# Optimization experiments

Hardware: AMD Instinct MI355X
Metric: run time of the kernel (lower is better)

## Reference

```python
import jax, jax.numpy as jnp
import numpy as np

D_MODEL = 768
N_LAYER = 4
VOCAB = 10000
N_MELS = 80
D_STATE = 16
D_CONV = 4
DT_RANK = 48          # ceil(768/16)
D_INNER = 1536        # expand * d_model
B_SZ, L_SEQ = 2, 1024


def rmsnorm(x, w, eps=1e-5):
    return x * jax.lax.rsqrt(jnp.mean(x * x, axis=-1, keepdims=True) + eps) * w


def causal_depthwise_conv(x, w, b):
    # x: (b, l, d_inner); w: (d_inner, 1, d_conv); torch Conv1d with padding=d_conv-1, truncated to l
    xc = jax.lax.conv_general_dilated(
        jnp.transpose(x, (0, 2, 1)), w, window_strides=(1,),
        padding=[(D_CONV - 1, 0)], dimension_numbers=('NCH', 'OIH', 'NCH'),
        feature_group_count=D_INNER)
    xc = xc + b[None, :, None]
    return jnp.transpose(xc, (0, 2, 1))


def selective_scan(u, dt, A, B, C, D):
    # u, dt: (b,l,d_in); A: (d_in,n); B,C: (b,l,n); D: (d_in,)
    dA = jnp.einsum('bld,dn->bldn', dt, A)
    dB_u = jnp.einsum('bld,bld,bln->bldn', dt, u, B)
    dA = jnp.clip(dA, -20, None)
    # shift dA by one step (exclusive cumulative decay), cumsum mode
    dA_shift = jnp.pad(dA[:, 1:], ((0, 0), (1, 0), (0, 0), (0, 0)))
    dA_cumsum = jnp.exp(jnp.cumsum(dA_shift, axis=1))
    x = jnp.cumsum(dB_u / (dA_cumsum + 1e-12), axis=1) * dA_cumsum
    y = jnp.einsum('bldn,bln->bld', x, C)
    return y + u * D


def mamba_block(x, rms_w, in_w, cw, cb, xp_w, dt_w, dt_b, A_log, Dp, out_w):
    h = rmsnorm(x, rms_w)
    xz = h @ in_w                       # (b,l,2*d_inner)
    xi, res = jnp.split(xz, 2, axis=-1)
    xi = jax.nn.silu(causal_depthwise_conv(xi, cw, cb))
    A = -jnp.exp(A_log.astype(jnp.float32))
    x_dbl = xi @ xp_w                   # (b,l,dt_rank+2n)
    delta = x_dbl[..., :DT_RANK]
    Bm = x_dbl[..., DT_RANK:DT_RANK + D_STATE]
    Cm = x_dbl[..., DT_RANK + D_STATE:]
    delta = jax.nn.softplus(delta @ dt_w + dt_b)
    y = selective_scan(xi, delta, A, Bm, Cm, Dp.astype(jnp.float32))
    y = y * jax.nn.silu(res)
    return y @ out_w + x


def setup_inputs():
    key = jax.random.key(0)
    ks = jax.random.split(key, 8)
    s = 0.02
    return {
        'input_ids': jax.random.randint(ks[0], (B_SZ, L_SEQ), 0, VOCAB),
        'embedding': jax.random.normal(ks[1], (VOCAB, D_MODEL), jnp.float32) * s,
        'rms_w': jnp.ones((N_LAYER, D_MODEL), jnp.float32),
        'in_proj_w': jax.random.normal(ks[2], (N_LAYER, D_MODEL, 2 * D_INNER), jnp.float32) * s,
        'conv_w': jax.random.normal(ks[3], (N_LAYER, D_INNER, 1, D_CONV), jnp.float32) * 0.1,
        'conv_b': jnp.zeros((N_LAYER, D_INNER), jnp.float32),
        'x_proj_w': jax.random.normal(ks[4], (N_LAYER, D_INNER, DT_RANK + 2 * D_STATE), jnp.float32) * s,
        'dt_proj_w': jax.random.normal(ks[5], (N_LAYER, DT_RANK, D_INNER), jnp.float32) * s,
        'dt_proj_b': jnp.zeros((N_LAYER, D_INNER), jnp.float32),
        'A_log': jnp.broadcast_to(jnp.log(jnp.arange(1, D_STATE + 1, dtype=jnp.float32)), (N_LAYER, D_INNER, D_STATE)) + 0.0,
        'D_param': jnp.ones((N_LAYER, D_INNER), jnp.float32),
        'out_proj_w': jax.random.normal(ks[6], (N_LAYER, D_INNER, D_MODEL), jnp.float32) * s,
        'norm_f_w': jnp.ones((D_MODEL,), jnp.float32),
        'head_w': jax.random.normal(ks[7], (D_MODEL, N_MELS), jnp.float32) * s,
    }


def reference(input_ids, embedding, rms_w, in_proj_w, conv_w, conv_b, x_proj_w,
              dt_proj_w, dt_proj_b, A_log, D_param, out_proj_w, norm_f_w, head_w):
    x = embedding[input_ids]            # (b,l,d)
    for i in range(N_LAYER):
        x = mamba_block(x, rms_w[i], in_proj_w[i], conv_w[i], conv_b[i],
                        x_proj_w[i], dt_proj_w[i], dt_proj_b[i], A_log[i],
                        D_param[i], out_proj_w[i])
    x = rmsnorm(x, norm_f_w)
    return x @ head_w                   # (b,l,n_mels)
```

## Files before the change

### kernel.cpp

```cpp
#include <hip/hip_runtime.h>
#include <hip/hip_bf16.h>
#include <math.h>

#define D_MODEL 768
#define N_LAYER 4
#define D_STATE 16
#define D_CONV  4
#define DT_RANK 48
#define D_INNER 1536
#define B_SZ    2
#define L_SEQ   1024
#define N_MELS  80
#define ROWS    (B_SZ * L_SEQ)

typedef __bf16 bf16x8 __attribute__((ext_vector_type(8)));
typedef float  f32x4  __attribute__((ext_vector_type(4)));

__device__ __forceinline__ float fast_exp2(float x) {
    float r; asm("v_exp_f32 %0, %1" : "=v"(r) : "v"(x)); return r;
}
__device__ __forceinline__ float fast_exp(float x) {
    return fast_exp2(x * 1.44269504f);
}
__device__ __forceinline__ float fast_rcp(float x) {
    float r; asm("v_rcp_f32 %0, %1" : "=v"(r) : "v"(x)); return r;
}
__device__ __forceinline__ float silu_f(float v) {
    return v * fast_rcp(1.0f + fast_exp(-v));
}
__device__ __forceinline__ float softplus_f(float v) {
    return fmaxf(v, 0.0f) + log1pf(expf(-fabsf(v)));
}
__device__ __forceinline__ unsigned short f2bf(float f) {
    unsigned int u = __float_as_uint(f);
    unsigned int r = (u + 0x7FFFu + ((u >> 16) & 1u)) >> 16;
    return (unsigned short)r;
}
__device__ __forceinline__ float bf2f(unsigned short v) {
    return __uint_as_float(((unsigned int)v) << 16);
}

__global__ void embed_kernel(const int* __restrict__ ids,
                             const float* __restrict__ emb,
                             float* __restrict__ x) {
    int i = blockIdx.x * 256 + threadIdx.x;
    if (i >= ROWS * D_MODEL) return;
    int r = i / D_MODEL, c = i - r * D_MODEL;
    x[i] = emb[(size_t)ids[r] * D_MODEL + c];
}

__global__ void rmsnorm_kernel(const float* __restrict__ x,
                               const float* __restrict__ w,
                               unsigned short* __restrict__ hb) {
    int row = blockIdx.x;
    const float* xr = x + (size_t)row * D_MODEL;
    int tid = threadIdx.x;
    float p = 0.f;
    for (int c = tid; c < D_MODEL; c += 256) { float v = xr[c]; p = fmaf(v, v, p); }
    for (int off = 32; off >= 1; off >>= 1) p += __shfl_down(p, off, 64);
    __shared__ float ws[4];
    int lane = tid & 63, wv = tid >> 6;
    if (lane == 0) ws[wv] = p;
    __syncthreads();
    if (tid == 0) ws[0] = ws[0] + ws[1] + ws[2] + ws[3];
    __syncthreads();
    float scale = 1.0f / sqrtf(ws[0] / (float)D_MODEL + 1e-5f);
    for (int c = tid; c < D_MODEL; c += 256)
        hb[(size_t)row * D_MODEL + c] = f2bf(xr[c] * scale * w[c]);
}

__global__ void prep_weights_kernel(const float* __restrict__ in_wi,
                                    const float* __restrict__ out_wi,
                                    const float* __restrict__ xp_wi,
                                    const float* __restrict__ dt_wi,
                                    unsigned short* __restrict__ wt_in,
                                    unsigned short* __restrict__ wt_out,
                                    unsigned short* __restrict__ xpT,
                                    unsigned short* __restrict__ dtwT) {
    __shared__ float t[32][33];
    int bx = blockIdx.x;
    int tid = threadIdx.x;
    if (bx < 3456) {
        const float* src; unsigned short* dst; int R, C, cy, cx;
        if (bx < 2304) {
            src = in_wi; dst = wt_in; R = D_MODEL; C = 2 * D_INNER;
            cy = bx / 96; cx = bx - cy * 96;
        } else {
            int tt = bx - 2304;
            src = out_wi; dst = wt_out; R = D_INNER; C = D_MODEL;
            cy = tt / 24; cx = tt - cy * 24;
        }
        int tx = tid & 31, ty = tid >> 5;
        int r0 = cy * 32, c0 = cx * 32;
#pragma unroll
        for (int i = 0; i < 4; i++)
            t[ty + i * 8][tx] = src[(size_t)(r0 + ty + i * 8) * C + c0 + tx];
        __syncthreads();
#pragma unroll
        for (int i = 0; i < 4; i++)
            dst[(size_t)(c0 + ty + i * 8) * R + r0 + tx] = f2bf(t[tx][ty + i * 8]);
    } else {
        int i = (bx - 3456) * 256 + tid;
        if (i < 80 * D_INNER) {
            int c = i / D_INNER, r = i - c * D_INNER;
            xpT[i] = f2bf(xp_wi[(size_t)r * 80 + c]);
        } else {
            int i2 = i - 80 * D_INNER;
            int c = i2 >> 6, r = i2 & 63;
            dtwT[i2] = (r < DT_RANK) ? f2bf(dt_wi[(size_t)r * D_INNER + c])
                                     : (unsigned short)0;
        }
    }
}

__global__ void transpose_u16_kernel(const unsigned short* __restrict__ src,
                                     unsigned short* __restrict__ dst,
                                     int R, int C) {
    __shared__ unsigned short t[32][34];
    int tx = threadIdx.x & 31, ty = threadIdx.x >> 5;
    int r0 = blockIdx.y * 32, c0 = blockIdx.x * 32;
#pragma unroll
    for (int i = 0; i < 4; i++)
        t[ty + i * 8][tx] = src[(size_t)(r0 + ty + i * 8) * C + c0 + tx];
    __syncthreads();
#pragma unroll
    for (int i = 0; i < 4; i++)
        dst[(size_t)(c0 + ty + i * 8) * R + r0 + tx] = t[tx][ty + i * 8];
}

__global__ void transpose_pad_bf16_kernel(const float* __restrict__ src,
                                          unsigned short* __restrict__ dst,
                                          int R, int C, int Rpad) {
    int i = blockIdx.x * 256 + threadIdx.x;
    if (i >= C * Rpad) return;
    int c = i / Rpad, r = i - c * Rpad;
    dst[i] = (r < R) ? f2bf(src[(size_t)r * C + c]) : (unsigned short)0;
}

__global__ void reduce_cvt_kernel(const float* __restrict__ part,
                                  float* __restrict__ xdbl,
                                  unsigned short* __restrict__ xdblb,
                                  int nsplit) {
    int i = blockIdx.x * 256 + threadIdx.x;
    if (i >= ROWS * 80) return;
    float s = 0.f;
    for (int k = 0; k < nsplit; k++) s += part[(size_t)k * ROWS * 80 + i];
    xdbl[i] = s;
    int r = i / 80, c = i - r * 80;
    if (c < DT_RANK) xdblb[r * 64 + c] = f2bf(s);
    else if (c >= 64) xdblb[r * 64 + c - 16] = 0;
}

__global__ void reduce_split_kernel(const float* __restrict__ part,
                                    float* __restrict__ dst,
                                    int MN, int nsplit) {
    int i = blockIdx.x * 256 + threadIdx.x;
    if (i >= MN) return;
    float s = 0.f;
    for (int k = 0; k < nsplit; k++) s += part[(size_t)k * MN + i];
    dst[i] = s;
}

__global__ __launch_bounds__(256) void mfma_gemm64(
        const unsigned short* __restrict__ A,
        const unsigned short* __restrict__ BT,
        const float* __restrict__ bias, const float* __restrict__ resid,
        float* __restrict__ Cf, unsigned short* __restrict__ Cb,
        int M, int N, int K, int ldc, int act, int bias_mode) {
    __shared__ unsigned short As[64][72];
    __shared__ unsigned short Bs[128][72];
    int tid = threadIdx.x;
    int row0 = blockIdx.y * 64, col0 = blockIdx.x * 128;
    int wave = tid >> 6, lane = tid & 63;
    int wr = (wave >> 1) * 32, wc = (wave & 1) * 64;
    int lm = lane & 15, lq = lane >> 4;
    int sr = tid >> 3, seg = tid & 7;
    const unsigned short* Ap0 = A  + (size_t)(row0 + sr) * K + seg * 8;
    const unsigned short* Ap1 = A  + (size_t)(row0 + 32 + sr) * K + seg * 8;
    const unsigned short* Bp0 = BT + (size_t)(col0 + sr) * K + seg * 8;
    const unsigned short* Bp1 = BT + (size_t)(col0 + 32 + sr) * K + seg * 8;
    const unsigned short* Bp2 = BT + (size_t)(col0 + 64 + sr) * K + seg * 8;
    const unsigned short* Bp3 = BT + (size_t)(col0 + 96 + sr) * K + seg * 8;
    f32x4 acc[2][4] = {};
    bf16x8 pa0 = *(const bf16x8*)Ap0;
    bf16x8 pa1 = *(const bf16x8*)Ap1;
    bf16x8 pb0 = *(const bf16x8*)Bp0;
    bf16x8 pb1 = *(const bf16x8*)Bp1;
    bf16x8 pb2 = *(const bf16x8*)Bp2;
    bf16x8 pb3 = *(const bf16x8*)Bp3;
    *(bf16x8*)&As[sr][seg * 8]      = pa0;
    *(bf16x8*)&As[32 + sr][seg * 8] = pa1;
    *(bf16x8*)&Bs[sr][seg * 8]      = pb0;
    *(bf16x8*)&Bs[32 + sr][seg * 8] = pb1;
    *(bf16x8*)&Bs[64 + sr][seg * 8] = pb2;
    *(bf16x8*)&Bs[96 + sr][seg * 8] = pb3;
    for (int k0 = 0; k0 < K; k0 += 64) {
        __syncthreads();
        bool more = (k0 + 64 < K);
        if (more) {
            pa0 = *(const bf16x8*)(Ap0 + k0 + 64);
            pa1 = *(const bf16x8*)(Ap1 + k0 + 64);
            pb0 = *(const bf16x8*)(Bp0 + k0 + 64);
            pb1 = *(const bf16x8*)(Bp1 + k0 + 64);
            pb2 = *(const bf16x8*)(Bp2 + k0 + 64);
            pb3 = *(const bf16x8*)(Bp3 + k0 + 64);
        }
#pragma unroll
        for (int ks = 0; ks < 2; ks++) {
            bf16x8 af[2], bfr[4];
#pragma unroll
            for (int i = 0; i < 2; i++)
                af[i] = *(const bf16x8*)&As[wr + i * 16 + lm][ks * 32 + lq * 8];
#pragma unroll
            for (int j = 0; j < 4; j++)
                bfr[j] = *(const bf16x8*)&Bs[wc + j * 16 + lm][ks * 32 + lq * 8];
#pragma unroll
            for (int i = 0; i < 2; i++)
#pragma unroll
                for (int j = 0; j < 4; j++)
                    acc[i][j] = __builtin_amdgcn_mfma_f32_16x16x32_bf16(af[i], bfr[j], acc[i][j], 0, 0, 0);
        }
        __syncthreads();
        if (more) {
            *(bf16x8*)&As[sr][seg * 8]      = pa0;
            *(bf16x8*)&As[32 + sr][seg * 8] = pa1;
            *(bf16x8*)&Bs[sr][seg * 8]      = pb0;
            *(bf16x8*)&Bs[32 + sr][seg * 8] = pb1;
            *(bf16x8*)&Bs[64 + sr][seg * 8] = pb2;
            *(bf16x8*)&Bs[96 + sr][seg * 8] = pb3;
        }
    }
#pragma unroll
    for (int i = 0; i < 2; i++) {
#pragma unroll
        for (int ii = 0; ii < 4; ii++) {
            int row = row0 + wr + i * 16 + lq * 4 + ii;
#pragma unroll
            for (int j = 0; j < 4; j++) {
                int col = col0 + wc + j * 16 + lm;
                float v = acc[i][j][ii];
                if (bias) v += bias[bias_mode ? row : col];
                if (act == 1) v = softplus_f(v);
                if (resid) v += resid[(size_t)row * ldc + col];
                if (Cf) Cf[(size_t)row * ldc + col] = v;
                else    Cb[(size_t)row * ldc + col] = f2bf(v);
            }
        }
    }
}

__global__ __launch_bounds__(256) void mfma_gemm32(
        const unsigned short* __restrict__ A,
        const unsigned short* __restrict__ BT,
        const float* __restrict__ bias, const float* __restrict__ resid,
        float* __restrict__ Cf, unsigned short* __restrict__ Cb,
        int M, int N, int K, int ldc, int act, int bias_mode) {
    __shared__ unsigned short As[32][72];
    __shared__ unsigned short Bs[128][72];
    int tid = threadIdx.x;
    int row0 = blockIdx.y * 32, col0 = blockIdx.x * 128;
    int wave = tid >> 6, lane = tid & 63;
    int wc = wave * 32;
    int lm = lane & 15, lq = lane >> 4;
    int sr = tid >> 3, seg = tid & 7;
    const unsigned short* Ap  = A  + (size_t)(row0 + sr) * K + seg * 8;
    const unsigned short* Bp0 = BT + (size_t)(col0 + sr) * K + seg * 8;
    const unsigned short* Bp1 = BT + (size_t)(col0 + 32 + sr) * K + seg * 8;
    const unsigned short* Bp2 = BT + (size_t)(col0 + 64 + sr) * K + seg * 8;
    const unsigned short* Bp3 = BT + (size_t)(col0 + 96 + sr) * K + seg * 8;
    f32x4 acc[2][2] = {};
    bf16x8 pa  = *(const bf16x8*)Ap;
    bf16x8 pb0 = *(const bf16x8*)Bp0;
    bf16x8 pb1 = *(const bf16x8*)Bp1;
    bf16x8 pb2 = *(const bf16x8*)Bp2;
    bf16x8 pb3 = *(const bf16x8*)Bp3;
    *(bf16x8*)&As[sr][seg * 8]      = pa;
    *(bf16x8*)&Bs[sr][seg * 8]      = pb0;
    *(bf16x8*)&Bs[32 + sr][seg * 8] = pb1;
    *(bf16x8*)&Bs[64 + sr][seg * 8] = pb2;
    *(bf16x8*)&Bs[96 + sr][seg * 8] = pb3;
    for (int k0 = 0; k0 < K; k0 += 64) {
        __syncthreads();
        bool more = (k0 + 64 < K);
        if (more) {
            pa  = *(const bf16x8*)(Ap  + k0 + 64);
            pb0 = *(const bf16x8*)(Bp0 + k0 + 64);
            pb1 = *(const bf16x8*)(Bp1 + k0 + 64);
            pb2 = *(const bf16x8*)(Bp2 + k0 + 64);
            pb3 = *(const bf16x8*)(Bp3 + k0 + 64);
        }
#pragma unroll
        for (int ks = 0; ks < 2; ks++) {
            bf16x8 af[2], bfr[2];
#pragma unroll
            for (int i = 0; i < 2; i++)
                af[i] = *(const bf16x8*)&As[i * 16 + lm][ks * 32 + lq * 8];
#pragma unroll
            for (int j = 0; j < 2; j++)
                bfr[j] = *(const bf16x8*)&Bs[wc + j * 16 + lm][ks * 32 + lq * 8];
#pragma unroll
            for (int i = 0; i < 2; i++)
#pragma unroll
                for (int j = 0; j < 2; j++)
                    acc[i][j] = __builtin_amdgcn_mfma_f32_16x16x32_bf16(af[i], bfr[j], acc[i][j], 0, 0, 0);
        }
        __syncthreads();
        if (more) {
            *(bf16x8*)&As[sr][seg * 8]      = pa;
            *(bf16x8*)&Bs[sr][seg * 8]      = pb0;
            *(bf16x8*)&Bs[32 + sr][seg * 8] = pb1;
            *(bf16x8*)&Bs[64 + sr][seg * 8] = pb2;
            *(bf16x8*)&Bs[96 + sr][seg * 8] = pb3;
        }
    }
#pragma unroll
    for (int i = 0; i < 2; i++) {
#pragma unroll
        for (int ii = 0; ii < 4; ii++) {
            int row = row0 + i * 16 + lq * 4 + ii;
#pragma unroll
            for (int j = 0; j < 2; j++) {
                int col = col0 + wc + j * 16 + lm;
                float v = acc[i][j][ii];
                if (bias) v += bias[bias_mode ? row : col];
                if (act == 1) v = softplus_f(v);
                if (resid) v += resid[(size_t)row * ldc + col];
                if (Cf) Cf[(size_t)row * ldc + col] = v;
                else    Cb[(size_t)row * ldc + col] = f2bf(v);
            }
        }
    }
}

__global__ __launch_bounds__(256) void mfma_skinny(
        const unsigned short* __restrict__ A,
        const unsigned short* __restrict__ BT,
        float* __restrict__ part,
        int M, int K, int kchunk) {
    constexpr int N = 80, NT = 5;
    __shared__ unsigned short As[128][40];
    __shared__ unsigned short Bs[80][40];
    int tid = threadIdx.x;
    int row0 = blockIdx.x * 128;
    int kb = blockIdx.y * kchunk, ke = kb + kchunk;
    float* myout = part + (size_t)blockIdx.y * M * N;
    int wave = tid >> 6, lane = tid & 63;
    int wr = wave * 32;
    int lm = lane & 15, lq = lane >> 4;
    int ar0 = tid >> 2, ar1 = (tid + 256) >> 2, aseg = tid & 3;
    const unsigned short* Ap0 = A + (size_t)(row0 + ar0) * K + aseg * 8;
    const unsigned short* Ap1 = A + (size_t)(row0 + ar1) * K + aseg * 8;
    const unsigned short* Bp0 = BT + (size_t)ar0 * K + aseg * 8;
    const unsigned short* Bp1 = BT + (size_t)ar1 * K + aseg * 8;
    bool haveB1 = (tid < 64);
    f32x4 acc[2][NT] = {};
    bf16x8 pa0 = *(const bf16x8*)(Ap0 + kb);
    bf16x8 pa1 = *(const bf16x8*)(Ap1 + kb);
    bf16x8 pb0 = *(const bf16x8*)(Bp0 + kb);
    bf16x8 pb1 = {};
    if (haveB1) pb1 = *(const bf16x8*)(Bp1 + kb);
    *(bf16x8*)&As[ar0][aseg * 8] = pa0;
    *(bf16x8*)&As[ar1][aseg * 8] = pa1;
    *(bf16x8*)&Bs[ar0][aseg * 8] = pb0;
    if (haveB1) *(bf16x8*)&Bs[ar1][aseg * 8] = pb1;
    for (int k0 = kb; k0 < ke; k0 += 32) {
        __syncthreads();
        bool more = (k0 + 32 < ke);
        if (more) {
            pa0 = *(const bf16x8*)(Ap0 + k0 + 32);
            pa1 = *(const bf16x8*)(Ap1 + k0 + 32);
            pb0 = *(const bf16x8*)(Bp0 + k0 + 32);
            if (haveB1) pb1 = *(const bf16x8*)(Bp1 + k0 + 32);
        }
        bf16x8 af[2], bfr[NT];
#pragma unroll
        for (int i = 0; i < 2; i++) af[i] = *(const bf16x8*)&As[wr + i * 16 + lm][lq * 8];
#pragma unroll
        for (int j = 0; j < NT; j++) bfr[j] = *(const bf16x8*)&Bs[j * 16 + lm][lq * 8];
#pragma unroll
        for (int i = 0; i < 2; i++)
#pragma unroll
            for (int j = 0; j < NT; j++)
                acc[i][j] = __builtin_amdgcn_mfma_f32_16x16x32_bf16(af[i], bfr[j], acc[i][j], 0, 0, 0);
        __syncthreads();
        if (more) {
            *(bf16x8*)&As[ar0][aseg * 8] = pa0;
            *(bf16x8*)&As[ar1][aseg * 8] = pa1;
            *(bf16x8*)&Bs[ar0][aseg * 8] = pb0;
            if (haveB1) *(bf16x8*)&Bs[ar1][aseg * 8] = pb1;
        }
    }
#pragma unroll
    for (int i = 0; i < 2; i++) {
#pragma unroll
        for (int ii = 0; ii < 4; ii++) {
            int row = row0 + wr + i * 16 + lq * 4 + ii;
#pragma unroll
            for (int j = 0; j < NT; j++) {
                int col = j * 16 + lm;
                myout[(size_t)row * N + col] = acc[i][j][ii];
            }
        }
    }
}

__global__ __launch_bounds__(256) void conv_silu_kernel(
        const unsigned short* __restrict__ xzb,
        const float* __restrict__ cw,
        const float* __restrict__ cb,
        unsigned short* __restrict__ ub,
        float* __restrict__ uT,
        unsigned short* __restrict__ resT) {
    __shared__ unsigned short s_xz[67][66];
    __shared__ float us[64][65];
    int tid = threadIdx.x;
    int d0 = blockIdx.x * 64, r0 = blockIdx.y * 64;
    bool atStart = (r0 & (L_SEQ - 1)) == 0;
    for (int idx = tid; idx < 67 * 64; idx += 256) {
        int rr = idx >> 6, cc2 = idx & 63;
        unsigned short v = 0;
        if (rr >= 3 || !atStart)
            v = xzb[(size_t)(r0 - 3 + rr) * (2 * D_INNER) + d0 + cc2];
        s_xz[rr][cc2] = v;
    }
    __syncthreads();
    int cc = tid & 63, ty = tid >> 6;
    const float* wp = cw + (size_t)(d0 + cc) * D_CONV;
    float w0 = wp[0], w1 = wp[1], w2 = wp[2], w3 = wp[3];
    float bb = cb[d0 + cc];
    for (int rr = ty; rr < 64; rr += 4) {
        float s = bb;
        s = fmaf(bf2f(s_xz[rr + 0][cc]), w0, s);
        s = fmaf(bf2f(s_xz[rr + 1][cc]), w1, s);
        s = fmaf(bf2f(s_xz[rr + 2][cc]), w2, s);
        s = fmaf(bf2f(s_xz[rr + 3][cc]), w3, s);
        float v = silu_f(s);
        ub[(size_t)(r0 + rr) * D_INNER + d0 + cc] = f2bf(v);
        us[rr][cc] = v;
    }
    __syncthreads();
    int tx = tid & 63, dy = tid >> 6;
    for (int dd = dy; dd < 64; dd += 4)
        uT[(size_t)(d0 + dd) * ROWS + r0 + tx] = us[tx][dd];
    __syncthreads();
    for (int idx = tid; idx < 64 * 64; idx += 256) {
        int rr = idx >> 6, cc2 = idx & 63;
        s_xz[rr][cc2] = xzb[(size_t)(r0 + rr) * (2 * D_INNER) + D_INNER + d0 + cc2];
    }
    __syncthreads();
    for (int dd = dy; dd < 64; dd += 4)
        resT[(size_t)(d0 + dd) * ROWS + r0 + tx] = s_xz[tx][dd];
}

__global__ __launch_bounds__(256) void scan_kernel(
        const float* __restrict__ deltaT,
        const float* __restrict__ uT,
        const float* __restrict__ xdbl,
        const unsigned short* __restrict__ resT,
        const float* __restrict__ A_log,
        const float* __restrict__ Dp,
        unsigned short* __restrict__ ygT) {
    int tid = threadIdx.x;
    int n = tid & 15, c = tid >> 4;
    int bd = blockIdx.x;
    int b = bd / D_INNER, d = bd - b * D_INNER;
    int row0 = b * L_SEQ;
    float a2 = -fast_exp(A_log[d * D_STATE + n]) * 1.44269504f;
    float Dd = Dp[d];
    __shared__ float2 s_du[L_SEQ + 16];
    __shared__ float cs1[16][17];
    __shared__ float cs2[16][17];
    __shared__ float gmv[16];
    const float* dptr = deltaT + (size_t)d * ROWS + row0;
    const float* uptr = uT + (size_t)d * ROWS + row0;
    for (int e = tid; e < L_SEQ; e += 256)
        s_du[e + (e >> 6)] = make_float2(dptr[e], uptr[e]);
    __syncthreads();
    {
        int l0 = c * 64, sb = l0 + c;
        bool notfirst = (c != 0);
        float sum = 0.f;
#pragma unroll 8
        for (int j = 0; j < 64; j++) {
            float dA = fmaxf(s_du[sb + j].x * a2, -28.8539008f);
            if (j > 0 || notfirst) sum += dA;
        }
        cs1[n][c] = sum;
    }
    __syncthreads();
    float cbase = 0.f;
    for (int cc = 0; cc < c; cc++) cbase += cs1[n][cc];
    float gm = cbase;
    gm = fmaxf(gm, __shfl_xor(gm, 1, 16));
    gm = fmaxf(gm, __shfl_xor(gm, 2, 16));
    gm = fmaxf(gm, __shfl_xor(gm, 4, 16));
    gm = fmaxf(gm, __shfl_xor(gm, 8, 16));
    if (n == 0) gmv[c] = gm;
    __syncthreads();
    int lc = 16;
    for (int cc = 1; cc < 16; cc++)
        if (gmv[cc] <= -150.0f) { lc = cc; break; }
    int clen = lc * 4;
    int l0b = c * clen;
    int lend = lc * 64;
    {
        float sum = 0.f;
        for (int j = 0; j < clen; j++) {
            int l = l0b + j;
            float dA = fmaxf(s_du[l + (l >> 6)].x * a2, -28.8539008f);
            if (l > 0) sum += dA;
        }
        cs1[n][c] = sum;
    }
    __syncthreads();
    float cbase_b = 0.f;
    for (int cc = 0; cc < c; cc++) cbase_b += cs1[n][cc];
    const float* xBbase = xdbl + (size_t)row0 * 80 + DT_RANK + n;
    {
        float Cacc = cbase_b, psum = 0.f;
        for (int j = 0; j < clen; j++) {
            int l = l0b + j;
            float2 du = s_du[l + (l >> 6)];
            float dA = fmaxf(du.x * a2, -28.8539008f);
            if (l > 0) Cacc += dA;
            float S = fast_exp2(Cacc);
            float r = fast_rcp(S + 1e-12f);
            psum = fmaf(du.x * du.y * xBbase[l * 80], r, psum);
        }
        cs2[n][c] = psum;
    }
    __syncthreads();
    float pbase = 0.f;
    for (int cc = 0; cc < c; cc++) pbase += cs2[n][cc];
    {
        float Cacc = cbase_b, P = pbase;
        for (int j = 0; j < clen; j++) {
            int l = l0b + j;
            float2 du = s_du[l + (l >> 6)];
            float dA = fmaxf(du.x * a2, -28.8539008f);
            if (l > 0) Cacc += dA;
            float S = fast_exp2(Cacc);
            float r = fast_rcp(S + 1e-12f);
            P = fmaf(du.x * du.y * xBbase[l * 80], r, P);
            float contrib = P * S * xBbase[l * 80 + 16];
            contrib += __shfl_xor(contrib, 1, 16);
            contrib += __shfl_xor(contrib, 2, 16);
            contrib += __shfl_xor(contrib, 4, 16);
            contrib += __shfl_xor(contrib, 8, 16);
            if (n == 0) s_du[l + (l >> 6)].x = contrib + du.y * Dd;
        }
    }
    __syncthreads();
    const unsigned short* rptr = resT + (size_t)d * ROWS + row0;
    unsigned short* yout = ygT + (size_t)d * ROWS + row0;
    for (int e = tid; e < L_SEQ; e += 256) {
        float2 v = s_du[e + (e >> 6)];
        float y = (e < lend) ? v.x : v.y * Dd;
        float res = bf2f(rptr[e]);
        yout[e] = f2bf(y * silu_f(res));
    }
}

extern "C" void kernel_launch(void* const* d_in, const int* in_sizes, int n_in,
                              void* d_out, int out_size, void* d_ws, size_t ws_size,
                              hipStream_t stream) {
    const int*   ids    = (const int*)d_in[0];
    const float* emb    = (const float*)d_in[1];
    const float* rms_w  = (const float*)d_in[2];
    const float* in_w   = (const float*)d_in[3];
    const float* conv_w = (const float*)d_in[4];
    const float* conv_b = (const float*)d_in[5];
    const float* xp_w   = (const float*)d_in[6];
    const float* dt_w   = (const float*)d_in[7];
    const float* dt_b   = (const float*)d_in[8];
    const float* A_log  = (const float*)d_in[9];
    const float* Dp     = (const float*)d_in[10];
    const float* out_w  = (const float*)d_in[11];
    const float* nf_w   = (const float*)d_in[12];
    const float* head_w = (const float*)d_in[13];
    float* out = (float*)d_out;

    char* base = (char*)d_ws;
    float*          x      = (float*)(base + 0);
    unsigned short* hb     = (unsigned short*)(base + 6291456);
    unsigned short* xzb    = (unsigned short*)(base + 9437184);
    unsigned short* ygT    = (unsigned short*)(base + 9437184);
    unsigned short* ygb    = (unsigned short*)(base + 15728640);
    float*          uT     = (float*)(base + 22020096);
    unsigned short* ub     = (unsigned short*)(base + 34603008);
    float*          xdbl   = (float*)(base + 40894464);
    unsigned short* xdblb  = (unsigned short*)(base + 41549824);
    float*          deltaT = (float*)(base + 41811968);
    float*          part   = (float*)(base + 41811968);
    unsigned short* resT   = (unsigned short*)(base + 54394880);
    unsigned short* wt_in  = (unsigned short*)(base + 60686336);
    unsigned short* wt_out = (unsigned short*)(base + 65404928);
    unsigned short* xpT    = (unsigned short*)(base + 67764224);
    unsigned short* dtwT   = (unsigned short*)(base + 68009984);
    unsigned short* headT  = (unsigned short*)(base + 68206592);

    embed_kernel<<<(ROWS * D_MODEL + 255) / 256, 256, 0, stream>>>(ids, emb, x);
    transpose_pad_bf16_kernel<<<(N_MELS * D_MODEL + 255) / 256, 256, 0, stream>>>(
        head_w, headT, D_MODEL, N_MELS, D_MODEL);

    for (int i = 0; i < N_LAYER; i++) {
        const float* in_wi   = in_w + (size_t)i * D_MODEL * 2 * D_INNER;
        const float* conv_wi = conv_w + (size_t)i * D_INNER * D_CONV;
        const float* conv_bi = conv_b + (size_t)i * D_INNER;
        const float* xp_wi   = xp_w + (size_t)i * D_INNER * (DT_RANK + 2 * D_STATE);
        const float* dt_wi   = dt_w + (size_t)i * DT_RANK * D_INNER;
        const float* dt_bi   = dt_b + (size_t)i * D_INNER;
        const float* A_li    = A_log + (size_t)i * D_INNER * D_STATE;
        const float* Dpi     = Dp + (size_t)i * D_INNER;
        const float* out_wi  = out_w + (size_t)i * D_INNER * D_MODEL;
        const float* rms_wi  = rms_w + (size_t)i * D_MODEL;

        prep_weights_kernel<<<4320, 256, 0, stream>>>(
            in_wi, out_wi, xp_wi, dt_wi, wt_in, wt_out, xpT, dtwT);

        rmsnorm_kernel<<<ROWS, 256, 0, stream>>>(x, rms_wi, hb);
        mfma_gemm64<<<dim3(2 * D_INNER / 128, ROWS / 64), 256, 0, stream>>>(
            hb, wt_in, nullptr, nullptr, nullptr, xzb,
            ROWS, 2 * D_INNER, D_MODEL, 2 * D_INNER, 0, 0);
        conv_silu_kernel<<<dim3(D_INNER / 64, ROWS / 64), 256, 0, stream>>>(
            xzb, conv_wi, conv_bi, ub, uT, resT);
        mfma_skinny<<<dim3(ROWS / 128, 16), 256, 0, stream>>>(
            ub, xpT, part, ROWS, D_INNER, D_INNER / 16);
        reduce_cvt_kernel<<<(ROWS * 80 + 255) / 256, 256, 0, stream>>>(
            part, xdbl, xdblb, 16);
        mfma_gemm32<<<dim3(ROWS / 128, D_INNER / 32), 256, 0, stream>>>(
            dtwT, xdblb, dt_bi, nullptr, deltaT, nullptr,
            D_INNER, ROWS, 64, ROWS, 1, 1);
        scan_kernel<<<B_SZ * D_INNER, 256, 0, stream>>>(
            deltaT, uT, xdbl, resT, A_li, Dpi, ygT);
        transpose_u16_kernel<<<dim3(ROWS / 32, D_INNER / 32), 256, 0, stream>>>(
            ygT, ygb, D_INNER, ROWS);
        mfma_gemm32<<<dim3(D_MODEL / 128, ROWS / 32), 256, 0, stream>>>(
            ygb, wt_out, nullptr, x, x, nullptr,
            ROWS, D_MODEL, D_INNER, D_MODEL, 0, 0);
    }

    rmsnorm_kernel<<<ROWS, 256, 0, stream>>>(x, nf_w, hb);
    mfma_skinny<<<dim3(ROWS / 128, 8), 256, 0, stream>>>(
        hb, headT, part, ROWS, D_MODEL, D_MODEL / 8);
    reduce_split_kernel<<<(ROWS * N_MELS + 255) / 256, 256, 0, stream>>>(
        part, out, ROWS * N_MELS, 8);
}
```

Before: 682.6 us.

## Read transposed operands directly in GEMMs and drop separate transpose kernels

The out-projection GEMM now reads the scan output in its transposed layout and transposes it into shared memory during the load. The x_proj skinny GEMM reads the fp32 transposed conv output and converts it to bf16 while staging. Together these remove the standalone transpose kernel and the extra bf16 row-major copy written by the conv kernel. The embedding gather and the head-weight transpose are also merged into one launch. The cost is scalar, strided shared-memory stores that may cause bank conflicts, and twice the global read bytes for the fp32 operand.

```diff
diff --git a/kernel.cpp b/kernel.cpp
--- a/kernel.cpp
+++ b/kernel.cpp
@@ -14,6 +14,7 @@
 #define ROWS    (B_SZ * L_SEQ)
 
 typedef __bf16 bf16x8 __attribute__((ext_vector_type(8)));
+typedef unsigned short u16x8 __attribute__((ext_vector_type(8)));
 typedef float  f32x4  __attribute__((ext_vector_type(4)));
 
 __device__ __forceinline__ float fast_exp2(float x) {
@@ -40,13 +41,22 @@
     return __uint_as_float(((unsigned int)v) << 16);
 }
 
-__global__ void embed_kernel(const int* __restrict__ ids,
-                             const float* __restrict__ emb,
-                             float* __restrict__ x) {
+__global__ void embed_head_kernel(const int* __restrict__ ids,
+                                  const float* __restrict__ emb,
+                                  float* __restrict__ x,
+                                  const float* __restrict__ head_w,
+                                  unsigned short* __restrict__ headT) {
     int i = blockIdx.x * 256 + threadIdx.x;
-    if (i >= ROWS * D_MODEL) return;
-    int r = i / D_MODEL, c = i - r * D_MODEL;
-    x[i] = emb[(size_t)ids[r] * D_MODEL + c];
+    if (i < ROWS * D_MODEL) {
+        int r = i / D_MODEL, c = i - r * D_MODEL;
+        x[i] = emb[(size_t)ids[r] * D_MODEL + c];
+    } else {
+        int j = i - ROWS * D_MODEL;
+        if (j < N_MELS * D_MODEL) {
+            int c = j / D_MODEL, r = j - c * D_MODEL;
+            headT[j] = f2bf(head_w[(size_t)r * N_MELS + c]);
+        }
+    }
 }
 
 __global__ void rmsnorm_kernel(const float* __restrict__ x,
@@ -111,30 +121,6 @@
                                      : (unsigned short)0;
         }
     }
-}
-
-__global__ void transpose_u16_kernel(const unsigned short* __restrict__ src,
-                                     unsigned short* __restrict__ dst,
-                                     int R, int C) {
-    __shared__ unsigned short t[32][34];
-    int tx = threadIdx.x & 31, ty = threadIdx.x >> 5;
-    int r0 = blockIdx.y * 32, c0 = blockIdx.x * 32;
-#pragma unroll
-    for (int i = 0; i < 4; i++)
-        t[ty + i * 8][tx] = src[(size_t)(r0 + ty + i * 8) * C + c0 + tx];
-    __syncthreads();
-#pragma unroll
-    for (int i = 0; i < 4; i++)
-        dst[(size_t)(c0 + ty + i * 8) * R + r0 + tx] = t[tx][ty + i * 8];
-}
-
-__global__ void transpose_pad_bf16_kernel(const float* __restrict__ src,
-                                          unsigned short* __restrict__ dst,
-                                          int R, int C, int Rpad) {
-    int i = blockIdx.x * 256 + threadIdx.x;
-    if (i >= C * Rpad) return;
-    int c = i / Rpad, r = i - c * Rpad;
-    dst[i] = (r < R) ? f2bf(src[(size_t)r * C + c]) : (unsigned short)0;
 }
 
 __global__ void reduce_cvt_kernel(const float* __restrict__ part,
@@ -249,6 +235,7 @@
     }
 }
 
+template<bool AT>
 __global__ __launch_bounds__(256) void mfma_gemm32(
         const unsigned short* __restrict__ A,
         const unsigned short* __restrict__ BT,
@@ -263,18 +250,27 @@
     int wc = wave * 32;
     int lm = lane & 15, lq = lane >> 4;
     int sr = tid >> 3, seg = tid & 7;
-    const unsigned short* Ap  = A  + (size_t)(row0 + sr) * K + seg * 8;
     const unsigned short* Bp0 = BT + (size_t)(col0 + sr) * K + seg * 8;
     const unsigned short* Bp1 = BT + (size_t)(col0 + 32 + sr) * K + seg * 8;
     const unsigned short* Bp2 = BT + (size_t)(col0 + 64 + sr) * K + seg * 8;
     const unsigned short* Bp3 = BT + (size_t)(col0 + 96 + sr) * K + seg * 8;
+    int akk = tid >> 2, arc = (tid & 3) * 8;
+    const unsigned short* ApT = AT ? (A + (size_t)akk * M + row0 + arc) : nullptr;
+    const unsigned short* Ap  = AT ? nullptr : (A + (size_t)(row0 + sr) * K + seg * 8);
     f32x4 acc[2][2] = {};
-    bf16x8 pa  = *(const bf16x8*)Ap;
+    u16x8 pa;
+    if (AT) pa = *(const u16x8*)ApT;
+    else    pa = *(const u16x8*)Ap;
     bf16x8 pb0 = *(const bf16x8*)Bp0;
     bf16x8 pb1 = *(const bf16x8*)Bp1;
     bf16x8 pb2 = *(const bf16x8*)Bp2;
     bf16x8 pb3 = *(const bf16x8*)Bp3;
-    *(bf16x8*)&As[sr][seg * 8]      = pa;
+    if (AT) {
+#pragma unroll
+        for (int j = 0; j < 8; j++) As[arc + j][akk] = pa[j];
+    } else {
+        *(u16x8*)&As[sr][seg * 8] = pa;
+    }
     *(bf16x8*)&Bs[sr][seg * 8]      = pb0;
     *(bf16x8*)&Bs[32 + sr][seg * 8] = pb1;
     *(bf16x8*)&Bs[64 + sr][seg * 8] = pb2;
@@ -283,7 +279,8 @@
         __syncthreads();
         bool more = (k0 + 64 < K);
         if (more) {
-            pa  = *(const bf16x8*)(Ap  + k0 + 64);
+            if (AT) pa = *(const u16x8*)(ApT + (size_t)(k0 + 64) * M);
+            else    pa = *(const u16x8*)(Ap + k0 + 64);
             pb0 = *(const bf16x8*)(Bp0 + k0 + 64);
             pb1 = *(const bf16x8*)(Bp1 + k0 + 64);
             pb2 = *(const bf16x8*)(Bp2 + k0 + 64);
@@ -306,7 +303,12 @@
         }
         __syncthreads();
         if (more) {
-            *(bf16x8*)&As[sr][seg * 8]      = pa;
+            if (AT) {
+#pragma unroll
+                for (int j = 0; j < 8; j++) As[arc + j][akk] = pa[j];
+            } else {
+                *(u16x8*)&As[sr][seg * 8] = pa;
+            }
             *(bf16x8*)&Bs[sr][seg * 8]      = pb0;
             *(bf16x8*)&Bs[32 + sr][seg * 8] = pb1;
             *(bf16x8*)&Bs[64 + sr][seg * 8] = pb2;
@@ -332,8 +334,10 @@
     }
 }
 
+template<bool AT>
 __global__ __launch_bounds__(256) void mfma_skinny(
         const unsigned short* __restrict__ A,
+        const float* __restrict__ AfT,
         const unsigned short* __restrict__ BT,
         float* __restrict__ part,
         int M, int K, int kchunk) {
@@ -348,27 +352,58 @@
     int wr = wave * 32;
     int lm = lane & 15, lq = lane >> 4;
     int ar0 = tid >> 2, ar1 = (tid + 256) >> 2, aseg = tid & 3;
-    const unsigned short* Ap0 = A + (size_t)(row0 + ar0) * K + aseg * 8;
-    const unsigned short* Ap1 = A + (size_t)(row0 + ar1) * K + aseg * 8;
+    const unsigned short* Ap0 = AT ? nullptr : (A + (size_t)(row0 + ar0) * K + aseg * 8);
+    const unsigned short* Ap1 = AT ? nullptr : (A + (size_t)(row0 + ar1) * K + aseg * 8);
+    int srl = tid >> 5, src4 = (tid & 31) * 4;
+    const float* Af0 = AT ? (AfT + (size_t)(srl + 0) * M + row0 + src4) : nullptr;
+    const float* Af1 = AT ? (AfT + (size_t)(srl + 8) * M + row0 + src4) : nullptr;
+    const float* Af2 = AT ? (AfT + (size_t)(srl + 16) * M + row0 + src4) : nullptr;
+    const float* Af3 = AT ? (AfT + (size_t)(srl + 24) * M + row0 + src4) : nullptr;
     const unsigned short* Bp0 = BT + (size_t)ar0 * K + aseg * 8;
     const unsigned short* Bp1 = BT + (size_t)ar1 * K + aseg * 8;
     bool haveB1 = (tid < 64);
     f32x4 acc[2][NT] = {};
-    bf16x8 pa0 = *(const bf16x8*)(Ap0 + kb);
-    bf16x8 pa1 = *(const bf16x8*)(Ap1 + kb);
+    bf16x8 pa0, pa1;
+    f32x4 qa0, qa1, qa2, qa3;
+    if (AT) {
+        qa0 = *(const f32x4*)(Af0 + (size_t)kb * M);
+        qa1 = *(const f32x4*)(Af1 + (size_t)kb * M);
+        qa2 = *(const f32x4*)(Af2 + (size_t)kb * M);
+        qa3 = *(const f32x4*)(Af3 + (size_t)kb * M);
+    } else {
+        pa0 = *(const bf16x8*)(Ap0 + kb);
+        pa1 = *(const bf16x8*)(Ap1 + kb);
+    }
     bf16x8 pb0 = *(const bf16x8*)(Bp0 + kb);
     bf16x8 pb1 = {};
     if (haveB1) pb1 = *(const bf16x8*)(Bp1 + kb);
-    *(bf16x8*)&As[ar0][aseg * 8] = pa0;
-    *(bf16x8*)&As[ar1][aseg * 8] = pa1;
+    if (AT) {
+#pragma unroll
+        for (int e = 0; e < 4; e++) {
+            As[src4 + e][srl]      = f2bf(qa0[e]);
+            As[src4 + e][srl + 8]  = f2bf(qa1[e]);
+            As[src4 + e][srl + 16] = f2bf(qa2[e]);
+            As[src4 + e][srl + 24] = f2bf(qa3[e]);
+        }
+    } else {
+        *(bf16x8*)&As[ar0][aseg * 8] = pa0;
+        *(bf16x8*)&As[ar1][aseg * 8] = pa1;
+    }
     *(bf16x8*)&Bs[ar0][aseg * 8] = pb0;
     if (haveB1) *(bf16x8*)&Bs[ar1][aseg * 8] = pb1;
     for (int k0 = kb; k0 < ke; k0 += 32) {
         __syncthreads();
         bool more = (k0 + 32 < ke);
         if (more) {
-            pa0 = *(const bf16x8*)(Ap0 + k0 + 32);
-            pa1 = *(const bf16x8*)(Ap1 + k0 + 32);
+            if (AT) {
+                qa0 = *(const f32x4*)(Af0 + (size_t)(k0 + 32) * M);
+                qa1 = *(const f32x4*)(Af1 + (size_t)(k0 + 32) * M);
+                qa2 = *(const f32x4*)(Af2 + (size_t)(k0 + 32) * M);
+                qa3 = *(const f32x4*)(Af3 + (size_t)(k0 + 32) * M);
+            } else {
+                pa0 = *(const bf16x8*)(Ap0 + k0 + 32);
+                pa1 = *(const bf16x8*)(Ap1 + k0 + 32);
+            }
             pb0 = *(const bf16x8*)(Bp0 + k0 + 32);
             if (haveB1) pb1 = *(const bf16x8*)(Bp1 + k0 + 32);
         }
@@ -384,8 +419,18 @@
                 acc[i][j] = __builtin_amdgcn_mfma_f32_16x16x32_bf16(af[i], bfr[j], acc[i][j], 0, 0, 0);
         __syncthreads();
         if (more) {
-            *(bf16x8*)&As[ar0][aseg * 8] = pa0;
-            *(bf16x8*)&As[ar1][aseg * 8] = pa1;
+            if (AT) {
+#pragma unroll
+                for (int e = 0; e < 4; e++) {
+                    As[src4 + e][srl]      = f2bf(qa0[e]);
+                    As[src4 + e][srl + 8]  = f2bf(qa1[e]);
+                    As[src4 + e][srl + 16] = f2bf(qa2[e]);
+                    As[src4 + e][srl + 24] = f2bf(qa3[e]);
+                }
+            } else {
+                *(bf16x8*)&As[ar0][aseg * 8] = pa0;
+                *(bf16x8*)&As[ar1][aseg * 8] = pa1;
+            }
             *(bf16x8*)&Bs[ar0][aseg * 8] = pb0;
             if (haveB1) *(bf16x8*)&Bs[ar1][aseg * 8] = pb1;
         }
@@ -408,7 +453,6 @@
         const unsigned short* __restrict__ xzb,
         const float* __restrict__ cw,
         const float* __restrict__ cb,
-        unsigned short* __restrict__ ub,
         float* __restrict__ uT,
         unsigned short* __restrict__ resT) {
     __shared__ unsigned short s_xz[67][66];
@@ -434,9 +478,7 @@
         s = fmaf(bf2f(s_xz[rr + 1][cc]), w1, s);
         s = fmaf(bf2f(s_xz[rr + 2][cc]), w2, s);
         s = fmaf(bf2f(s_xz[rr + 3][cc]), w3, s);
-        float v = silu_f(s);
-        ub[(size_t)(r0 + rr) * D_INNER + d0 + cc] = f2bf(v);
-        us[rr][cc] = v;
+        us[rr][cc] = silu_f(s);
     }
     __syncthreads();
     int tx = tid & 63, dy = tid >> 6;
@@ -585,9 +627,7 @@
     unsigned short* hb     = (unsigned short*)(base + 6291456);
     unsigned short* xzb    = (unsigned short*)(base + 9437184);
     unsigned short* ygT    = (unsigned short*)(base + 9437184);
-    unsigned short* ygb    = (unsigned short*)(base + 15728640);
     float*          uT     = (float*)(base + 22020096);
-    unsigned short* ub     = (unsigned short*)(base + 34603008);
     float*          xdbl   = (float*)(base + 40894464);
     unsigned short* xdblb  = (unsigned short*)(base + 41549824);
     float*          deltaT = (float*)(base + 41811968);
@@ -599,9 +639,8 @@
     unsigned short* dtwT   = (unsigned short*)(base + 68009984);
     unsigned short* headT  = (unsigned short*)(base + 68206592);
 
-    embed_kernel<<<(ROWS * D_MODEL + 255) / 256, 256, 0, stream>>>(ids, emb, x);
-    transpose_pad_bf16_kernel<<<(N_MELS * D_MODEL + 255) / 256, 256, 0, stream>>>(
-        head_w, headT, D_MODEL, N_MELS, D_MODEL);
+    embed_head_kernel<<<(ROWS * D_MODEL + N_MELS * D_MODEL + 255) / 256, 256, 0, stream>>>(
+        ids, emb, x, head_w, headT);
 
     for (int i = 0; i < N_LAYER; i++) {
         const float* in_wi   = in_w + (size_t)i * D_MODEL * 2 * D_INNER;
@@ -623,26 +662,24 @@
             hb, wt_in, nullptr, nullptr, nullptr, xzb,
             ROWS, 2 * D_INNER, D_MODEL, 2 * D_INNER, 0, 0);
         conv_silu_kernel<<<dim3(D_INNER / 64, ROWS / 64), 256, 0, stream>>>(
-            xzb, conv_wi, conv_bi, ub, uT, resT);
-        mfma_skinny<<<dim3(ROWS / 128, 16), 256, 0, stream>>>(
-            ub, xpT, part, ROWS, D_INNER, D_INNER / 16);
+            xzb, conv_wi, conv_bi, uT, resT);
+        mfma_skinny<true><<<dim3(ROWS / 128, 16), 256, 0, stream>>>(
+            nullptr, uT, xpT, part, ROWS, D_INNER, D_INNER / 16);
         reduce_cvt_kernel<<<(ROWS * 80 + 255) / 256, 256, 0, stream>>>(
             part, xdbl, xdblb, 16);
-        mfma_gemm32<<<dim3(ROWS / 128, D_INNER / 32), 256, 0, stream>>>(
+        mfma_gemm32<false><<<dim3(ROWS / 128, D_INNER / 32), 256, 0, stream>>>(
             dtwT, xdblb, dt_bi, nullptr, deltaT, nullptr,
             D_INNER, ROWS, 64, ROWS, 1, 1);
         scan_kernel<<<B_SZ * D_INNER, 256, 0, stream>>>(
             deltaT, uT, xdbl, resT, A_li, Dpi, ygT);
-        transpose_u16_kernel<<<dim3(ROWS / 32, D_INNER / 32), 256, 0, stream>>>(
-            ygT, ygb, D_INNER, ROWS);
-        mfma_gemm32<<<dim3(D_MODEL / 128, ROWS / 32), 256, 0, stream>>>(
-            ygb, wt_out, nullptr, x, x, nullptr,
+        mfma_gemm32<true><<<dim3(D_MODEL / 128, ROWS / 32), 256, 0, stream>>>(
+            ygT, wt_out, nullptr, x, x, nullptr,
             ROWS, D_MODEL, D_INNER, D_MODEL, 0, 0);
     }
 
     rmsnorm_kernel<<<ROWS, 256, 0, stream>>>(x, nf_w, hb);
-    mfma_skinny<<<dim3(ROWS / 128, 8), 256, 0, stream>>>(
-        hb, headT, part, ROWS, D_MODEL, D_MODEL / 8);
+    mfma_skinny<false><<<dim3(ROWS / 128, 8), 256, 0, stream>>>(
+        hb, nullptr, headT, part, ROWS, D_MODEL, D_MODEL / 8);
     reduce_split_kernel<<<(ROWS * N_MELS + 255) / 256, 256, 0, stream>>>(
         part, out, ROWS * N_MELS, 8);
 }
```

After: 681.3 us. About the same (-0.2%).
